# Kernel optimization log

Measured on AMD Instinct MI355X. Metric: run time of the kernel, lower is better.

Reference implementation:

```python
import jax, jax.numpy as jnp
import numpy as np

L, B, S, H, NH, DH, I, MAXP, NL = 4, 8, 512, 1024, 32, 32, 4096, 512, 20
EPS = 1e-12


def setup_inputs() -> dict:
    key = jax.random.key(0)
    ks = jax.random.split(key, 12)
    sc = 0.02
    w = lambda k, shape: jax.random.normal(k, shape, jnp.float32) * sc
    p = {}
    p['hidden_states'] = jax.random.normal(ks[0], (B, S, H), jnp.float32)
    p['attention_mask'] = jnp.ones((B, S), jnp.float32)
    p['Wq'] = w(ks[1], (L, H, H)); p['bq'] = jnp.zeros((L, H), jnp.float32)
    p['Wk'] = w(ks[2], (L, H, H)); p['bk'] = jnp.zeros((L, H), jnp.float32)
    p['Wv'] = w(ks[3], (L, H, H)); p['bv'] = jnp.zeros((L, H), jnp.float32)
    p['Wo'] = w(ks[4], (L, H, H)); p['bo'] = jnp.zeros((L, H), jnp.float32)
    p['ln1_g'] = jnp.ones((L, H), jnp.float32); p['ln1_b'] = jnp.zeros((L, H), jnp.float32)
    p['W1'] = w(ks[5], (L, H, I)); p['b1'] = jnp.zeros((L, I), jnp.float32)
    p['W2'] = w(ks[6], (L, I, H)); p['b2'] = jnp.zeros((L, H), jnp.float32)
    p['ln2_g'] = jnp.ones((L, H), jnp.float32); p['ln2_b'] = jnp.zeros((L, H), jnp.float32)
    p['rel_emb'] = w(ks[7], (L, 2 * MAXP - 1, DH))
    p['pool_W'] = w(ks[8], (3 * H, H)); p['pool_b'] = jnp.zeros((H,), jnp.float32)
    p['pool_ln_g'] = jnp.ones((H,), jnp.float32); p['pool_ln_b'] = jnp.zeros((H,), jnp.float32)
    p['cls_W'] = w(ks[9], (H, NL)); p['cls_b'] = jnp.zeros((NL,), jnp.float32)
    return p


def _ln(x, g, b):
    mu = jnp.mean(x, -1, keepdims=True)
    var = jnp.mean(jnp.square(x - mu), -1, keepdims=True)
    return (x - mu) * jax.lax.rsqrt(var + EPS) * g + b


def reference(hidden_states, attention_mask, Wq, bq, Wk, bk, Wv, bv, Wo, bo,
              ln1_g, ln1_b, W1, b1, W2, b2, ln2_g, ln2_b, rel_emb,
              pool_W, pool_b, pool_ln_g, pool_ln_b, cls_W, cls_b):
    b, s, h = hidden_states.shape
    # extended additive attention mask (0 -> -1e9)
    mask_add = (1.0 - attention_mask)[:, None, None, :] * -1e9
    pos = jnp.arange(s)
    rel_idx = pos[:, None] - pos[None, :] + MAXP - 1  # [s, s] in [0, 2*MAXP-2]
    x = hidden_states
    for l in range(L):
        heads = lambda t: t.reshape(b, s, NH, DH).transpose(0, 2, 1, 3)
        q = heads(x @ Wq[l] + bq[l])
        k = heads(x @ Wk[l] + bk[l])
        v = heads(x @ Wv[l] + bv[l])
        # learned relative-position bias; note head_size == num_heads by construction
        rel = rel_emb[l][rel_idx].transpose(2, 0, 1)  # [DH==NH, s, s]
        scores = jnp.einsum('bhqd,bhkd->bhqk', q, k) + rel[None]
        scores = scores / np.float32(np.sqrt(DH)) + mask_add
        probs = jax.nn.softmax(scores, axis=-1)
        ctx = jnp.einsum('bhqk,bhkd->bhqd', probs, v).transpose(0, 2, 1, 3).reshape(b, s, h)
        x = _ln(ctx @ Wo[l] + bo[l] + x, ln1_g[l], ln1_b[l])
        inner = jax.nn.gelu(x @ W1[l] + b1[l], approximate=False) @ W2[l] + b2[l]
        x = _ln(x + inner, ln2_g[l], ln2_b[l])
    # AdvancedPooling: mean + max + first token
    m = attention_mask[..., None]
    mean_pool = jnp.sum(x * m, axis=1) / jnp.sum(attention_mask, axis=1, keepdims=True)
    max_pool = jnp.max(x + (1.0 - m) * -1e9, axis=1)
    pooled = jnp.concatenate([mean_pool, max_pool, x[:, 0]], axis=-1)
    pooled = _ln(pooled @ pool_W + pool_b, pool_ln_g, pool_ln_b)
    return pooled @ cls_W + cls_b
```

## Files before the change

### kernel.cpp

```cpp
#include <hip/hip_runtime.h>
#include <math.h>

typedef __attribute__((ext_vector_type(8))) _Float16 f16x8;
typedef __attribute__((ext_vector_type(4))) float f32x4;

__device__ __forceinline__ ushort f2h(float x) {
  union { _Float16 h; ushort u; } c;
  c.h = (_Float16)x;
  return c.u;
}
__device__ __forceinline__ void gl_lds16(const ushort* g, ushort* l) {
  __builtin_amdgcn_global_load_lds(
      (const __attribute__((address_space(1))) unsigned int*)g,
      (__attribute__((address_space(3))) unsigned int*)l, 16, 0, 0);
}
__device__ __forceinline__ f32x4 mfma16(f16x8 a, f16x8 b, f32x4 c) {
  return __builtin_amdgcn_mfma_f32_16x16x32_f16(a, b, c, 0, 0, 0);
}

__device__ __forceinline__ float block_reduce_sum(float v, float* sb) {
#pragma unroll
  for (int o = 32; o > 0; o >>= 1) v += __shfl_down(v, o, 64);
  const int t = threadIdx.x;
  if ((t & 63) == 0) sb[t >> 6] = v;
  __syncthreads();
  v = sb[0] + sb[1] + sb[2] + sb[3];
  __syncthreads();
  return v;
}

__global__ __launch_bounds__(256) void acast(const float* __restrict__ X,
                                             ushort* __restrict__ H, int n4) {
  const int i = blockIdx.x * 256 + threadIdx.x;
  if (i >= n4) return;
  const float4 x = ((const float4*)X)[i];
  ushort4 h;
  h.x = f2h(x.x); h.y = f2h(x.y); h.z = f2h(x.z); h.w = f2h(x.w);
  ((ushort4*)H)[i] = h;
}

__global__ __launch_bounds__(256) void concat3(const float* __restrict__ a,
                                               const float* __restrict__ b,
                                               const float* __restrict__ c,
                                               float* __restrict__ o) {
  const int i = blockIdx.x * 256 + threadIdx.x;
  o[i] = i < 1024 ? a[i] : (i < 2048 ? b[i - 1024] : c[i - 2048]);
}

__global__ __launch_bounds__(256) void wcast_t(const float* __restrict__ W,
                                               ushort* __restrict__ T,
                                               int K, int N) {
  __shared__ float s[32][33];
  const int tx = threadIdx.x & 31, ty = threadIdx.x >> 5;
  const int n0 = blockIdx.x * 32, k0 = blockIdx.y * 32;
#pragma unroll
  for (int i = 0; i < 4; ++i)
    s[ty + i * 8][tx] = W[(size_t)(k0 + ty + i * 8) * N + n0 + tx];
  __syncthreads();
#pragma unroll
  for (int i = 0; i < 4; ++i) {
    const int n = ty + i * 8;
    T[(size_t)(n0 + n) * K + k0 + tx] = f2h(s[tx][n]);
  }
}

__global__ __launch_bounds__(256) void wcast_t3(const float* __restrict__ W0,
                                                const float* __restrict__ W1,
                                                const float* __restrict__ W2,
                                                ushort* __restrict__ T) {
  __shared__ float s[32][33];
  const float* W = blockIdx.z == 0 ? W0 : (blockIdx.z == 1 ? W1 : W2);
  ushort* Tp = T + (size_t)blockIdx.z * 1024 * 1024;
  const int tx = threadIdx.x & 31, ty = threadIdx.x >> 5;
  const int n0 = blockIdx.x * 32, k0 = blockIdx.y * 32;
#pragma unroll
  for (int i = 0; i < 4; ++i)
    s[ty + i * 8][tx] = W[(size_t)(k0 + ty + i * 8) * 1024 + n0 + tx];
  __syncthreads();
#pragma unroll
  for (int i = 0; i < 4; ++i) {
    const int n = ty + i * 8;
    Tp[(size_t)(n0 + n) * 1024 + k0 + tx] = f2h(s[tx][n]);
  }
}

template <int EPI, int KSPLIT>
__global__ __launch_bounds__(256, 2) void gemm_mfma(
    const ushort* __restrict__ A, const ushort* __restrict__ B,
    const float* __restrict__ bias, const float* __restrict__ res,
    float* __restrict__ C, float* __restrict__ C2, ushort* __restrict__ O,
    int M, int N, int K) {
  __shared__ __align__(16) ushort sA[2][4096], sB[2][4096];
  const int t = threadIdx.x, w = t >> 6, lane = t & 63;
  const int llo = lane & 15, lhi = lane >> 4;
  const int wm = w >> 1, wn = w & 1;
  const int z = (KSPLIT > 1) ? blockIdx.z : 0;
  const int Ks = K / KSPLIT;

  const int gx = gridDim.x;
  int wg = blockIdx.y * gx + blockIdx.x;
  const int nwg = gx * gridDim.y;
  wg = (wg & 7) * (nwg >> 3) + (wg >> 3);
  const int bm = (wg / gx) * 128, bn = (wg % gx) * 128;

  const ushort* pA0 = A + (size_t)(bm + lane) * K + w * 8 + z * Ks;
  const ushort* pA1 = pA0 + (size_t)64 * K;
  const ushort* pB0 = B + (size_t)(bn + lane) * K + w * 8 + z * Ks;
  const ushort* pB1 = pB0 + (size_t)64 * K;

  auto STAGE = [&](int buf, int k0) {
    gl_lds16(pA0 + k0, &sA[buf][w * 1024]);
    gl_lds16(pA1 + k0, &sA[buf][w * 1024 + 512]);
    gl_lds16(pB0 + k0, &sB[buf][w * 1024]);
    gl_lds16(pB1 + k0, &sB[buf][w * 1024 + 512]);
  };

  f32x4 acc[4][4] = {};
  const int NT = Ks >> 5;
  STAGE(0, 0);
  __syncthreads();
  int cur = 0;
  for (int kt = 0; kt < NT; ++kt) {
    if (kt + 1 < NT) STAGE(cur ^ 1, (kt + 1) << 5);
    f16x8 a[4], bfr[4];
#pragma unroll
    for (int f = 0; f < 4; ++f) {
      a[f] = *(const f16x8*)&sA[cur][lhi * 1024 + (wm * 64 + f * 16 + llo) * 8];
      bfr[f] = *(const f16x8*)&sB[cur][lhi * 1024 + (wn * 64 + f * 16 + llo) * 8];
    }
#pragma unroll
    for (int fm = 0; fm < 4; ++fm)
#pragma unroll
      for (int fn = 0; fn < 4; ++fn)
        acc[fm][fn] = mfma16(a[fm], bfr[fn], acc[fm][fn]);
    __syncthreads();
    cur ^= 1;
  }

#pragma unroll
  for (int fm = 0; fm < 4; ++fm) {
    const int row0 = bm + wm * 64 + fm * 16 + lhi * 4;
#pragma unroll
    for (int fn = 0; fn < 4; ++fn) {
      const int col = bn + wn * 64 + fn * 16 + llo;
      const float bc = bias[col];
      if (EPI == 5) {
        if (col < 2048) {
          const size_t base = (size_t)(col >> 10) * (4096 * 1024) + (col & 1023);
#pragma unroll
          for (int r = 0; r < 4; ++r)
            O[base + (size_t)(row0 + r) * 1024] = f2h(acc[fm][fn][r] + bc);
        } else {
          const int c = col - 2048;
          ushort4 vh;
#pragma unroll
          for (int r = 0; r < 4; ++r) ((ushort*)&vh)[r] = f2h(acc[fm][fn][r] + bc);
          const size_t o = (size_t)8 * 1024 * 1024 +
              ((size_t)(((row0 >> 9) * 32 + (c >> 5)) * 32 + (c & 31))) * 512 +
              (row0 & 511);
          *(ushort4*)(O + o) = vh;
        }
      } else if (EPI == 2) {
#pragma unroll
        for (int r = 0; r < 4; ++r) {
          const size_t o = (size_t)(row0 + r) * N + col;
          if (KSPLIT == 1 || z == 0)
            C[o] = acc[fm][fn][r] + bc + res[o];
          else
            C2[o] = acc[fm][fn][r];
        }
      } else {
#pragma unroll
        for (int r = 0; r < 4; ++r) {
          const size_t o = (size_t)(row0 + r) * N + col;
          float v = acc[fm][fn][r] + bc;
          v = 0.5f * v * (1.f + erff(v * 0.70710678118654752f));
          O[o] = f2h(v);
        }
      }
    }
  }
}

__global__ __launch_bounds__(512, 2) void attn_mfma(
    const ushort* __restrict__ Qg, const ushort* __restrict__ Kg,
    const ushort* __restrict__ Vg, const float* __restrict__ mask,
    const float* __restrict__ rel_l, ushort* __restrict__ Cg) {
  __shared__ __align__(16) ushort sK[16384], sV[16384];
  __shared__ __align__(16) ushort sP[5120];
  __shared__ float rel_s[1024];
  __shared__ float madd[512];

  const int h = blockIdx.x, b = blockIdx.y, z = blockIdx.z;
  const int t = threadIdx.x, w = t >> 6, lane = t & 63;
  const int llo = lane & 15, lhi = lane >> 4;
  const float SCALE = 0.17677669529663687f;

#pragma unroll
  for (int it = 0; it < 4; ++it) {
    const int task = t + it * 512;
    const int s = task >> 2, oct = task & 3;
    const size_t g = (size_t)(b * 512 + s) * 1024 + h * 32 + oct * 8;
    *(uint4*)&sK[oct * 4096 + s * 8] = *(const uint4*)(Kg + g);
  }
#pragma unroll
  for (int it = 0; it < 4; ++it) {
    const int task = t + it * 512;
    const int d = task >> 6, ko = task & 63;
    const size_t g = (size_t)((b * 32 + h) * 32 + d) * 512 + ko * 8;
    *(uint4*)&sV[ko * 256 + d * 8] = *(const uint4*)(Vg + g);
  }
  for (int i = t; i < 1023; i += 512) rel_s[i] = rel_l[(size_t)i * 32 + h];
  for (int i = t; i < 512; i += 512) madd[i] = (1.f - mask[b * 512 + i]) * -1e9f;
  __syncthreads();

  uint* wP = (uint*)(sP + w * 640 + llo * 40);
  const ushort* rP = sP + w * 640 + llo * 40;

  for (int qt = 0; qt < 2; ++qt) {
    const int q = z * 256 + w * 32 + qt * 16 + llo;
    const size_t qg = (size_t)(b * 512 + q) * 1024 + h * 32 + lhi * 8;
    const f16x8 fQ = *(const f16x8*)(Qg + qg);
    float m = -INFINITY, l = 0.f;
    f32x4 acc0 = {0.f, 0.f, 0.f, 0.f};
    f32x4 acc1 = {0.f, 0.f, 0.f, 0.f};

    for (int kt2 = 0; kt2 < 16; ++kt2) {
      float p[8];
      float tm = -INFINITY;
#pragma unroll
      for (int sub = 0; sub < 2; ++sub) {
        const int kt = kt2 * 2 + sub;
        const f16x8 fK = *(const f16x8*)&sK[lhi * 4096 + (kt * 16 + llo) * 8];
        f32x4 s4 = {0.f, 0.f, 0.f, 0.f};
        s4 = mfma16(fK, fQ, s4);
#pragma unroll
        for (int r = 0; r < 4; ++r) {
          const int k = kt * 16 + lhi * 4 + r;
          const float sv = (s4[r] + rel_s[q - k + 511]) * SCALE + madd[k];
          p[sub * 4 + r] = sv;
          tm = fmaxf(tm, sv);
        }
      }
      tm = fmaxf(tm, __shfl_xor(tm, 16));
      tm = fmaxf(tm, __shfl_xor(tm, 32));
      const float nm = fmaxf(m, tm);
      const float sc = __expf(m - nm);
      float ts = 0.f;
#pragma unroll
      for (int i = 0; i < 8; ++i) {
        p[i] = __expf(p[i] - nm);
        ts += p[i];
      }
      ts += __shfl_xor(ts, 16);
      ts += __shfl_xor(ts, 32);
      l = l * sc + ts;
      m = nm;
      acc0 *= sc;
      acc1 *= sc;
#pragma unroll
      for (int sub = 0; sub < 2; ++sub) {
        wP[sub * 8 + lhi * 2 + 0] =
            (uint)f2h(p[sub * 4 + 0]) | ((uint)f2h(p[sub * 4 + 1]) << 16);
        wP[sub * 8 + lhi * 2 + 1] =
            (uint)f2h(p[sub * 4 + 2]) | ((uint)f2h(p[sub * 4 + 3]) << 16);
      }
      const f16x8 fP = *(const f16x8*)(rP + lhi * 8);
      const int vb = (kt2 * 4 + lhi) * 256;
      const f16x8 fV0 = *(const f16x8*)&sV[vb + llo * 8];
      const f16x8 fV1 = *(const f16x8*)&sV[vb + (16 + llo) * 8];
      acc0 = mfma16(fV0, fP, acc0);
      acc1 = mfma16(fV1, fP, acc1);
    }

    const float invl = 1.f / l;
    const size_t ob = (size_t)(b * 512 + q) * 1024 + h * 32;
    ushort4 oh;
#pragma unroll
    for (int r = 0; r < 4; ++r) ((ushort*)&oh)[r] = f2h(acc0[r] * invl);
    *(ushort4*)(Cg + ob + lhi * 4) = oh;
#pragma unroll
    for (int r = 0; r < 4; ++r) ((ushort*)&oh)[r] = f2h(acc1[r] * invl);
    *(ushort4*)(Cg + ob + 16 + lhi * 4) = oh;
  }
}

__global__ __launch_bounds__(256) void ln_kernel(
    const float* __restrict__ X, const float* __restrict__ X2,
    const float* __restrict__ g, const float* __restrict__ bt,
    float* __restrict__ out, ushort* __restrict__ O) {
  __shared__ float sb[4];
  const int row = blockIdx.x, t = threadIdx.x;
  float4 x = *(const float4*)&X[(size_t)row * 1024 + t * 4];
  if (X2) {
    const float4 y = *(const float4*)&X2[(size_t)row * 1024 + t * 4];
    x.x += y.x; x.y += y.y; x.z += y.z; x.w += y.w;
  }
  const float s = block_reduce_sum(x.x + x.y + x.z + x.w, sb);
  const float mu = s * (1.f / 1024.f);
  const float dx = x.x - mu, dy = x.y - mu, dz = x.z - mu, dw = x.w - mu;
  const float ss = block_reduce_sum(dx * dx + dy * dy + dz * dz + dw * dw, sb);
  const float rs = rsqrtf(ss * (1.f / 1024.f) + 1e-12f);
  const float4 gv = *(const float4*)&g[t * 4];
  const float4 bv = *(const float4*)&bt[t * 4];
  float4 o;
  o.x = dx * rs * gv.x + bv.x;
  o.y = dy * rs * gv.y + bv.y;
  o.z = dz * rs * gv.z + bv.z;
  o.w = dw * rs * gv.w + bv.w;
  *(float4*)&out[(size_t)row * 1024 + t * 4] = o;
  if (O) {
    ushort4 vh;
    vh.x = f2h(o.x); vh.y = f2h(o.y); vh.z = f2h(o.z); vh.w = f2h(o.w);
    *(ushort4*)&O[(size_t)row * 1024 + t * 4] = vh;
  }
}

__global__ __launch_bounds__(128) void pool_part(
    const float* __restrict__ X, const float* __restrict__ mask,
    float* __restrict__ psum, float* __restrict__ pmax,
    float* __restrict__ pcnt) {
  const int cb = blockIdx.x, b = blockIdx.y, sb = blockIdx.z;
  const int col = cb * 128 + threadIdx.x;
  float sum = 0.f, mx = -INFINITY, cnt = 0.f;
  for (int i = 0; i < 128; ++i) {
    const int s = sb * 128 + i;
    const float v = X[(size_t)(b * 512 + s) * 1024 + col];
    const float mk = mask[b * 512 + s];
    sum = fmaf(v, mk, sum);
    cnt += mk;
    mx = fmaxf(mx, v + (1.f - mk) * -1e9f);
  }
  psum[(size_t)(sb * 8 + b) * 1024 + col] = sum;
  pmax[(size_t)(sb * 8 + b) * 1024 + col] = mx;
  if (cb == 0 && threadIdx.x == 0) pcnt[sb * 8 + b] = cnt;
}

__global__ __launch_bounds__(256) void pool_fin(
    const float* __restrict__ X, const float* __restrict__ psum,
    const float* __restrict__ pmax, const float* __restrict__ pcnt,
    float* __restrict__ pooled) {
  const int idx = blockIdx.x * 256 + threadIdx.x;
  const int b = idx >> 10, col = idx & 1023;
  float s = 0.f, m = -INFINITY, c = 0.f;
#pragma unroll
  for (int sb = 0; sb < 4; ++sb) {
    s += psum[(size_t)(sb * 8 + b) * 1024 + col];
    m = fmaxf(m, pmax[(size_t)(sb * 8 + b) * 1024 + col]);
    c += pcnt[sb * 8 + b];
  }
  pooled[(size_t)b * 3072 + col] = s / c;
  pooled[(size_t)b * 3072 + 1024 + col] = m;
  pooled[(size_t)b * 3072 + 2048 + col] = X[(size_t)(b * 512) * 1024 + col];
}

__global__ __launch_bounds__(256) void pgemm_part(
    const float* __restrict__ P, const float* __restrict__ W,
    float* __restrict__ part) {
  __shared__ float sP[8][192];
  __shared__ float sacc[256][9];
  const int nb = blockIdx.x, kb = blockIdx.y;
  const int t = threadIdx.x;
  const int k0 = kb * 192, n0 = nb * 64;
  for (int i = t; i < 1536; i += 256)
    sP[i / 192][i % 192] = P[(size_t)(i / 192) * 3072 + k0 + i % 192];
  __syncthreads();
  const int n = t & 63, kq = t >> 6;
  float acc[8] = {};
  for (int kk = 0; kk < 48; ++kk) {
    const int k = kq * 48 + kk;
    const float wv = W[(size_t)(k0 + k) * 1024 + n0 + n];
#pragma unroll
    for (int b = 0; b < 8; ++b) acc[b] = fmaf(sP[b][k], wv, acc[b]);
  }
#pragma unroll
  for (int b = 0; b < 8; ++b) sacc[t][b] = acc[b];
  __syncthreads();
  for (int p = t; p < 512; p += 256) {
    const int b = p >> 6, nn = p & 63;
    const float v = sacc[nn][b] + sacc[64 + nn][b] + sacc[128 + nn][b] +
                    sacc[192 + nn][b];
    part[((size_t)kb * 8 + b) * 1024 + n0 + nn] = v;
  }
}

__global__ __launch_bounds__(256) void pgemm_fin(
    const float* __restrict__ part, const float* __restrict__ bias,
    float* __restrict__ out) {
  const int idx = blockIdx.x * 256 + threadIdx.x;
  const int b = idx >> 10, n = idx & 1023;
  float v = bias[n];
#pragma unroll
  for (int kb = 0; kb < 16; ++kb) v += part[((size_t)kb * 8 + b) * 1024 + n];
  out[(size_t)b * 1024 + n] = v;
}

__global__ __launch_bounds__(64) void cls_kernel(
    const float* __restrict__ X, const float* __restrict__ W,
    const float* __restrict__ bias, float* __restrict__ out) {
  const int n = blockIdx.x, b = blockIdx.y, lane = threadIdx.x;
  float a = 0.f;
#pragma unroll
  for (int i = 0; i < 16; ++i) {
    const int k = lane + i * 64;
    a = fmaf(X[(size_t)b * 1024 + k], W[(size_t)k * 20 + n], a);
  }
#pragma unroll
  for (int o = 32; o > 0; o >>= 1) a += __shfl_down(a, o, 64);
  if (lane == 0) out[b * 20 + n] = a + bias[n];
}

extern "C" void kernel_launch(void* const* d_in, const int* in_sizes, int n_in,
                              void* d_out, int out_size, void* d_ws, size_t ws_size,
                              hipStream_t stream) {
  const float* hs    = (const float*)d_in[0];
  const float* amask = (const float*)d_in[1];
  const float* Wq    = (const float*)d_in[2];
  const float* bq    = (const float*)d_in[3];
  const float* Wk    = (const float*)d_in[4];
  const float* bk    = (const float*)d_in[5];
  const float* Wv    = (const float*)d_in[6];
  const float* bv    = (const float*)d_in[7];
  const float* Wo    = (const float*)d_in[8];
  const float* bo    = (const float*)d_in[9];
  const float* ln1g  = (const float*)d_in[10];
  const float* ln1b  = (const float*)d_in[11];
  const float* W1    = (const float*)d_in[12];
  const float* b1    = (const float*)d_in[13];
  const float* W2    = (const float*)d_in[14];
  const float* b2    = (const float*)d_in[15];
  const float* ln2g  = (const float*)d_in[16];
  const float* ln2b  = (const float*)d_in[17];
  const float* rel   = (const float*)d_in[18];
  const float* poolW = (const float*)d_in[19];
  const float* poolb = (const float*)d_in[20];
  const float* plng  = (const float*)d_in[21];
  const float* plnb  = (const float*)d_in[22];
  const float* clsW  = (const float*)d_in[23];
  const float* clsb  = (const float*)d_in[24];

  char* W = (char*)d_ws;
  const size_t MB = (size_t)1 << 20;
  const size_t QK = (size_t)4096 * 1024;
  float* buf_t  = (float*)(W + 0 * MB);
  float* buf_t2 = (float*)(W + 16 * MB);
  float* buf_h1 = (float*)(W + 32 * MB);
  float* buf_x  = (float*)(W + 48 * MB);
  ushort* PL  = (ushort*)(W + 64 * MB);
  ushort* CTX = (ushort*)(W + 88 * MB);
  ushort* Xp  = CTX;
  ushort* H1  = (ushort*)(W + 96 * MB);
  ushort* F1  = (ushort*)(W + 104 * MB);
  ushort* Wt  = (ushort*)(W + 136 * MB);
  float* bcat = (float*)(W + 142 * MB);
  float* sm   = (float*)(W + 143 * MB);
  float* pooled  = sm;
  float* pool_h  = pooled + 8 * 3072;
  float* pool_h2 = pool_h + 8 * 1024;
  float* pcnt    = pool_h2 + 8 * 1024;
  float* psum    = pcnt + 64;
  float* pmax    = psum + 4 * 8 * 1024;
  float* pgpart  = pmax + 4 * 8 * 1024;

  const int n4act = (4096 * 1024) / 4;
  const dim3 gQKV(3072 / 128, 32);
  const dim3 gF1(4096 / 128, 32);
  const dim3 gKS(1024 / 128, 32, 2);
  const dim3 wsQ3(32, 32, 3);

  acast<<<n4act / 256, 256, 0, stream>>>(hs, Xp, n4act);

  const float* x_in = hs;
  for (int l = 0; l < 4; ++l) {
    const float* Wq_l = Wq + (size_t)l * 1024 * 1024;
    const float* Wk_l = Wk + (size_t)l * 1024 * 1024;
    const float* Wv_l = Wv + (size_t)l * 1024 * 1024;
    const float* Wo_l = Wo + (size_t)l * 1024 * 1024;
    const float* W1_l = W1 + (size_t)l * 1024 * 4096;
    const float* W2_l = W2 + (size_t)l * 4096 * 1024;

    concat3<<<12, 256, 0, stream>>>(bq + l * 1024, bk + l * 1024, bv + l * 1024, bcat);
    wcast_t3<<<wsQ3, 256, 0, stream>>>(Wq_l, Wk_l, Wv_l, Wt);
    gemm_mfma<5, 1><<<gQKV, 256, 0, stream>>>(Xp, Wt, bcat, nullptr, nullptr,
                                              nullptr, PL, 4096, 3072, 1024);

    attn_mfma<<<dim3(32, 8, 2), 512, 0, stream>>>(
        PL, PL + QK, PL + 2 * QK, amask, rel + (size_t)l * 1023 * 32, CTX);

    wcast_t<<<dim3(32, 32), 256, 0, stream>>>(Wo_l, Wt, 1024, 1024);
    gemm_mfma<2, 2><<<gKS, 256, 0, stream>>>(CTX, Wt, bo + l * 1024, x_in,
                                             buf_t, buf_t2, nullptr, 4096, 1024, 1024);
    ln_kernel<<<4096, 256, 0, stream>>>(buf_t, buf_t2, ln1g + l * 1024,
                                        ln1b + l * 1024, buf_h1, H1);

    wcast_t<<<dim3(4096 / 32, 1024 / 32), 256, 0, stream>>>(W1_l, Wt, 1024, 4096);
    gemm_mfma<1, 1><<<gF1, 256, 0, stream>>>(H1, Wt, b1 + l * 4096, nullptr,
                                             nullptr, nullptr, F1, 4096, 4096, 1024);
    wcast_t<<<dim3(1024 / 32, 4096 / 32), 256, 0, stream>>>(W2_l, Wt, 4096, 1024);
    gemm_mfma<2, 2><<<gKS, 256, 0, stream>>>(F1, Wt, b2 + l * 1024, buf_h1,
                                             buf_t, buf_t2, nullptr, 4096, 1024, 4096);
    ln_kernel<<<4096, 256, 0, stream>>>(buf_t, buf_t2, ln2g + l * 1024,
                                        ln2b + l * 1024, buf_x, Xp);
    x_in = buf_x;
  }

  pool_part<<<dim3(8, 8, 4), 128, 0, stream>>>(buf_x, amask, psum, pmax, pcnt);
  pool_fin<<<32, 256, 0, stream>>>(buf_x, psum, pmax, pcnt, pooled);
  pgemm_part<<<dim3(16, 16), 256, 0, stream>>>(pooled, poolW, pgpart);
  pgemm_fin<<<32, 256, 0, stream>>>(pgpart, poolb, pool_h);
  ln_kernel<<<8, 256, 0, stream>>>(pool_h, nullptr, plng, plnb, pool_h2, nullptr);
  cls_kernel<<<dim3(20, 8), 64, 0, stream>>>(pool_h2, clsW, clsb, (float*)d_out);
}
```

Baseline: 1.333 ms.

## Add 256x256-tile, 512-thread GEMM kernel for QKV and FFN1 projections

Introduces a gemm256 kernel with 256x256 output tiles, 8 waves per block and 8x4 MFMA fragments per wave, and uses it for the QKV and FFN-up GEMMs in place of the 128x128 kernel. Larger tiles raise arithmetic intensity and cut redundant global/LDS traffic per output element. The cost is a much smaller grid (192 and 256 blocks on a 256-CU part), more accumulator registers per thread and 64KB of LDS per block, which may lower occupancy and leave the GPU underfilled. The older kernel's epilogue is trimmed to only the residual path it still serves.

```diff
diff --git a/kernel.cpp b/kernel.cpp
--- a/kernel.cpp
+++ b/kernel.cpp
@@ -81,6 +81,94 @@
   for (int i = 0; i < 4; ++i) {
     const int n = ty + i * 8;
     Tp[(size_t)(n0 + n) * 1024 + k0 + tx] = f2h(s[tx][n]);
+  }
+}
+
+template <int EPI>
+__global__ __launch_bounds__(512, 2) void gemm256(
+    const ushort* __restrict__ A, const ushort* __restrict__ B,
+    const float* __restrict__ bias, float* __restrict__ C,
+    ushort* __restrict__ O, int M, int N, int K) {
+  __shared__ __align__(16) ushort sA[2][8192], sB[2][8192];
+  const int t = threadIdx.x, w = t >> 6, lane = t & 63;
+  const int llo = lane & 15, lhi = lane >> 4;
+  const int wm = w >> 2, wn = w & 3;
+  const int rb = w >> 2, ko = w & 3;
+
+  const int gx = gridDim.x;
+  int wg = blockIdx.y * gx + blockIdx.x;
+  const int nwg = gx * gridDim.y;
+  wg = (wg & 7) * (nwg >> 3) + (wg >> 3);
+  const int bm = (wg / gx) * 256, bn = (wg % gx) * 256;
+
+  const ushort* pA0 = A + (size_t)(bm + rb * 128 + lane) * K + ko * 8;
+  const ushort* pA1 = pA0 + (size_t)64 * K;
+  const ushort* pB0 = B + (size_t)(bn + rb * 128 + lane) * K + ko * 8;
+  const ushort* pB1 = pB0 + (size_t)64 * K;
+
+  auto STAGE = [&](int buf, int k0) {
+    gl_lds16(pA0 + k0, &sA[buf][ko * 2048 + rb * 1024]);
+    gl_lds16(pA1 + k0, &sA[buf][ko * 2048 + rb * 1024 + 512]);
+    gl_lds16(pB0 + k0, &sB[buf][ko * 2048 + rb * 1024]);
+    gl_lds16(pB1 + k0, &sB[buf][ko * 2048 + rb * 1024 + 512]);
+  };
+
+  f32x4 acc[8][4] = {};
+  const int NT = K >> 5;
+  STAGE(0, 0);
+  __syncthreads();
+  int cur = 0;
+  for (int kt = 0; kt < NT; ++kt) {
+    if (kt + 1 < NT) STAGE(cur ^ 1, (kt + 1) << 5);
+    f16x8 a[8], bfr[4];
+#pragma unroll
+    for (int f = 0; f < 8; ++f)
+      a[f] = *(const f16x8*)&sA[cur][lhi * 2048 + (wm * 128 + f * 16 + llo) * 8];
+#pragma unroll
+    for (int f = 0; f < 4; ++f)
+      bfr[f] = *(const f16x8*)&sB[cur][lhi * 2048 + (wn * 64 + f * 16 + llo) * 8];
+#pragma unroll
+    for (int fm = 0; fm < 8; ++fm)
+#pragma unroll
+      for (int fn = 0; fn < 4; ++fn)
+        acc[fm][fn] = mfma16(a[fm], bfr[fn], acc[fm][fn]);
+    __syncthreads();
+    cur ^= 1;
+  }
+
+#pragma unroll
+  for (int fm = 0; fm < 8; ++fm) {
+    const int row0 = bm + wm * 128 + fm * 16 + lhi * 4;
+#pragma unroll
+    for (int fn = 0; fn < 4; ++fn) {
+      const int col = bn + wn * 64 + fn * 16 + llo;
+      const float bc = bias[col];
+      if (EPI == 5) {
+        if (col < 2048) {
+          const size_t base = (size_t)(col >> 10) * (4096 * 1024) + (col & 1023);
+#pragma unroll
+          for (int r = 0; r < 4; ++r)
+            O[base + (size_t)(row0 + r) * 1024] = f2h(acc[fm][fn][r] + bc);
+        } else {
+          const int c = col - 2048;
+          ushort4 vh;
+#pragma unroll
+          for (int r = 0; r < 4; ++r) ((ushort*)&vh)[r] = f2h(acc[fm][fn][r] + bc);
+          const size_t o = (size_t)8 * 1024 * 1024 +
+              ((size_t)(((row0 >> 9) * 32 + (c >> 5)) * 32 + (c & 31))) * 512 +
+              (row0 & 511);
+          *(ushort4*)(O + o) = vh;
+        }
+      } else {
+#pragma unroll
+        for (int r = 0; r < 4; ++r) {
+          const size_t o = (size_t)(row0 + r) * N + col;
+          float v = acc[fm][fn][r] + bc;
+          v = 0.5f * v * (1.f + erff(v * 0.70710678118654752f));
+          O[o] = f2h(v);
+        }
+      }
+    }
   }
 }
 
@@ -144,39 +232,13 @@
     for (int fn = 0; fn < 4; ++fn) {
       const int col = bn + wn * 64 + fn * 16 + llo;
       const float bc = bias[col];
-      if (EPI == 5) {
-        if (col < 2048) {
-          const size_t base = (size_t)(col >> 10) * (4096 * 1024) + (col & 1023);
-#pragma unroll
-          for (int r = 0; r < 4; ++r)
-            O[base + (size_t)(row0 + r) * 1024] = f2h(acc[fm][fn][r] + bc);
-        } else {
-          const int c = col - 2048;
-          ushort4 vh;
-#pragma unroll
-          for (int r = 0; r < 4; ++r) ((ushort*)&vh)[r] = f2h(acc[fm][fn][r] + bc);
-          const size_t o = (size_t)8 * 1024 * 1024 +
-              ((size_t)(((row0 >> 9) * 32 + (c >> 5)) * 32 + (c & 31))) * 512 +
-              (row0 & 511);
-          *(ushort4*)(O + o) = vh;
-        }
-      } else if (EPI == 2) {
-#pragma unroll
-        for (int r = 0; r < 4; ++r) {
-          const size_t o = (size_t)(row0 + r) * N + col;
-          if (KSPLIT == 1 || z == 0)
-            C[o] = acc[fm][fn][r] + bc + res[o];
-          else
-            C2[o] = acc[fm][fn][r];
-        }
-      } else {
-#pragma unroll
-        for (int r = 0; r < 4; ++r) {
-          const size_t o = (size_t)(row0 + r) * N + col;
-          float v = acc[fm][fn][r] + bc;
-          v = 0.5f * v * (1.f + erff(v * 0.70710678118654752f));
-          O[o] = f2h(v);
-        }
+#pragma unroll
+      for (int r = 0; r < 4; ++r) {
+        const size_t o = (size_t)(row0 + r) * N + col;
+        if (KSPLIT == 1 || z == 0)
+          C[o] = acc[fm][fn][r] + bc + res[o];
+        else
+          C2[o] = acc[fm][fn][r];
       }
     }
   }
@@ -463,8 +525,8 @@
   float* pgpart  = pmax + 4 * 8 * 1024;
 
   const int n4act = (4096 * 1024) / 4;
-  const dim3 gQKV(3072 / 128, 32);
-  const dim3 gF1(4096 / 128, 32);
+  const dim3 gQKV(3072 / 256, 4096 / 256);
+  const dim3 gF1(4096 / 256, 4096 / 256);
   const dim3 gKS(1024 / 128, 32, 2);
   const dim3 wsQ3(32, 32, 3);
 
@@ -481,8 +543,8 @@
 
     concat3<<<12, 256, 0, stream>>>(bq + l * 1024, bk + l * 1024, bv + l * 1024, bcat);
     wcast_t3<<<wsQ3, 256, 0, stream>>>(Wq_l, Wk_l, Wv_l, Wt);
-    gemm_mfma<5, 1><<<gQKV, 256, 0, stream>>>(Xp, Wt, bcat, nullptr, nullptr,
-                                              nullptr, PL, 4096, 3072, 1024);
+    gemm256<5><<<gQKV, 512, 0, stream>>>(Xp, Wt, bcat, nullptr, PL,
+                                         4096, 3072, 1024);
 
     attn_mfma<<<dim3(32, 8, 2), 512, 0, stream>>>(
         PL, PL + QK, PL + 2 * QK, amask, rel + (size_t)l * 1023 * 32, CTX);
@@ -494,8 +556,8 @@
                                         ln1b + l * 1024, buf_h1, H1);
 
     wcast_t<<<dim3(4096 / 32, 1024 / 32), 256, 0, stream>>>(W1_l, Wt, 1024, 4096);
-    gemm_mfma<1, 1><<<gF1, 256, 0, stream>>>(H1, Wt, b1 + l * 4096, nullptr,
-                                             nullptr, nullptr, F1, 4096, 4096, 1024);
+    gemm256<1><<<gF1, 512, 0, stream>>>(H1, Wt, b1 + l * 4096, nullptr, F1,
+                                        4096, 4096, 1024);
     wcast_t<<<dim3(1024 / 32, 4096 / 32), 256, 0, stream>>>(W2_l, Wt, 4096, 1024);
     gemm_mfma<2, 2><<<gKS, 256, 0, stream>>>(F1, Wt, b2 + l * 1024, buf_h1,
                                              buf_t, buf_t2, nullptr, 4096, 1024, 4096);
```

Result: no change. 1.351 ms (+1.3%).
